# Optimization experiments

Measured on AMD Instinct MI355X. Metric: run time of the kernel, lower is better.

Reference implementation:

```python
import jax, jax.numpy as jnp
import numpy as np

GROUPSIZE = 128
IN_F, OUT_F = 4096, 11008
TOKENS = 512


def setup_inputs() -> dict:
    key = jax.random.key(0)
    k1, k2, k3, k4, k5 = jax.random.split(key, 5)
    x = jax.random.normal(k1, (TOKENS, IN_F), dtype=jnp.float32)
    # packed 4-bit codes: two nibbles per byte, stored as int32 in [0, 256)
    qweight = jax.random.randint(k2, (OUT_F * IN_F // 2,), 0, 256, dtype=jnp.int32)
    n_groups = OUT_F * IN_F // GROUPSIZE
    scales = jax.random.uniform(k3, (n_groups, 1), dtype=jnp.float32) * 0.02 + 1e-3
    zeros = jax.random.uniform(k4, (n_groups, 1), dtype=jnp.float32) * 15.0
    bias = jax.random.normal(k5, (OUT_F,), dtype=jnp.float32)
    return {"x": x, "qweight": qweight, "scales": scales, "zeros": zeros, "bias": bias}


def _dequant_w4(qweight, scales, zeros, dtype):
    # python_decompress: high nibble then low nibble, each in [0,16)
    hi = (qweight >> 4) % 16
    lo = qweight % 16
    codes = jnp.stack([hi, lo], axis=-1).reshape(-1, GROUPSIZE).astype(dtype)
    # group-wise dequant: (code - zero) * scale, zeros/scales are (n_groups, 1)
    w = (codes - zeros.astype(dtype)) * scales.astype(dtype)
    return w.reshape(OUT_F, IN_F)


def reference(x, qweight, scales, zeros, bias):
    w = _dequant_w4(qweight, scales, zeros, x.dtype)  # [out, in]
    return x @ w.T + bias
```

## Files before the change

kernel.cpp:

```cpp
#include <hip/hip_runtime.h>

#define GROUPSIZE 128
#define IN_F 4096
#define OUT_F 11008
#define TOKENS 512
#define N_GROUPS (OUT_F * IN_F / GROUPSIZE)
#define NGK (IN_F / GROUPSIZE)

#define BM 64
#define BN 128
#define BK 64
#define NTHREADS 256
#define NT_G (IN_F / BK)
#define NT_H (NT_G / 2)
#define NTILES_N (OUT_F / BN)

typedef _Float16 half8  __attribute__((ext_vector_type(8)));
typedef _Float16 half2v __attribute__((ext_vector_type(2)));
typedef float    f32x4  __attribute__((ext_vector_type(4)));
typedef int      ivec4  __attribute__((ext_vector_type(4)));

__device__ __forceinline__ int swz(int r, int k) {
    return ((r << 6) + k) ^ ((r & 7) << 3);
}

__device__ __forceinline__ void glds16(const _Float16* g, _Float16* l) {
    __builtin_amdgcn_global_load_lds(
        (const __attribute__((address_space(1))) void*)g,
        (__attribute__((address_space(3))) void*)l, 16, 0, 0);
}

__device__ __forceinline__ unsigned pack4(ivec4 q) {
    unsigned p01 = __builtin_amdgcn_perm((unsigned)q[1], (unsigned)q[0], 0x0C0C0400u);
    unsigned p23 = __builtin_amdgcn_perm((unsigned)q[3], (unsigned)q[2], 0x0C0C0400u);
    return __builtin_amdgcn_perm(p23, p01, 0x05040100u);
}

__device__ __forceinline__ half8 dqp(unsigned p, uint2 sz) {
    unsigned A4 = (p << 4) & 0xF0F0F0F0u;
    unsigned Bn =  p       & 0xF0F0F0F0u;
    unsigned t01 = __builtin_amdgcn_perm(A4, Bn, 0x05010400u);
    unsigned t23 = __builtin_amdgcn_perm(A4, Bn, 0x07030602u);
    const unsigned k54 = 0x54545454u;
    unsigned u0 = __builtin_amdgcn_perm(t01, k54, 0x00050004u);
    unsigned u1 = __builtin_amdgcn_perm(t01, k54, 0x00070006u);
    unsigned u2 = __builtin_amdgcn_perm(t23, k54, 0x00050004u);
    unsigned u3 = __builtin_amdgcn_perm(t23, k54, 0x00070006u);
    half2v S  = __builtin_bit_cast(half2v, sz.x);
    half2v Bv = __builtin_bit_cast(half2v, sz.y);
    union { half8 h; half2v p2[4]; } r;
    r.p2[0] = __builtin_bit_cast(half2v, u0) * S + Bv;
    r.p2[1] = __builtin_bit_cast(half2v, u1) * S + Bv;
    r.p2[2] = __builtin_bit_cast(half2v, u2) * S + Bv;
    r.p2[3] = __builtin_bit_cast(half2v, u3) * S + Bv;
    return r.h;
}

__global__ __launch_bounds__(256)
void cvt_x_kernel(const float* __restrict__ x, _Float16* __restrict__ x16) {
    size_t i = ((size_t)blockIdx.x * 256 + threadIdx.x) * 8;
    f32x4 a = *(const f32x4*)(x + i);
    f32x4 b = *(const f32x4*)(x + i + 4);
    half8 h;
    h[0]=(_Float16)a[0]; h[1]=(_Float16)a[1]; h[2]=(_Float16)a[2]; h[3]=(_Float16)a[3];
    h[4]=(_Float16)b[0]; h[5]=(_Float16)b[1]; h[6]=(_Float16)b[2]; h[7]=(_Float16)b[3];
    *(half8*)(x16 + i) = h;
}

__global__ __launch_bounds__(256)
void szpack_kernel(const float* __restrict__ s, const float* __restrict__ z,
                   uint2* __restrict__ szt) {
    int g = blockIdx.x * 256 + threadIdx.x;
    if (g >= N_GROUPS) return;
    int row = g / NGK, gk = g % NGK;
    _Float16 S = (_Float16)s[g];
    _Float16 B = (_Float16)(-(64.0f + z[g]) * (float)S);
    unsigned short su = __builtin_bit_cast(unsigned short, S);
    unsigned short bu = __builtin_bit_cast(unsigned short, B);
    uint2 r;
    r.x = ((unsigned)su << 16) | su;
    r.y = ((unsigned)bu << 16) | bu;
    szt[(size_t)gk * OUT_F + row] = r;
}

__global__ __launch_bounds__(256)
void out_init_kernel(const float* __restrict__ bias, float* __restrict__ out) {
    size_t i = ((size_t)blockIdx.x * 256 + threadIdx.x) * 4;
    int col = (int)(i % OUT_F);
    *(f32x4*)(out + i) = *(const f32x4*)(bias + col);
}

__global__ __launch_bounds__(NTHREADS, 4)
void qlinear_main(const _Float16* __restrict__ x16,
                  const int*   __restrict__ qw,
                  const uint2* __restrict__ szt,
                  float*       __restrict__ out)
{
    __shared__ __align__(16) _Float16 As[2][BM * BK];
    __shared__ __align__(16) unsigned Qs[2][BN * BK / 8];

    const int bid = blockIdx.x;
    const int xcd = bid & 7;
    const int sgrp = bid >> 3;
    const int n_t = 11 * xcd + (sgrp >> 4);
    const int sub = sgrp & 15;
    const int m_t = sub & 7;
    const int kh  = sub >> 3;
    if (n_t >= NTILES_N) return;
    const int n0 = n_t * BN, m0 = m_t * BM;
    const int t0 = kh * NT_H;

    const int tid = threadIdx.x;
    const int wv = tid >> 6, ln = tid & 63;

    const int s8 = tid & 7, r0 = tid >> 3;
    const int* qg = qw + (size_t)(n0 + r0) * (IN_F / 2) + (size_t)t0 * 32 + s8 * 4;
    const int dwp = s8 ^ ((r0 >> 2) & 3);

    const int ar  = wv * 16 + (ln >> 3);
    const int gsw = (ln & 7) ^ ((ln >> 3) & 7);
    const _Float16* ag = x16 + (size_t)(m0 + ar) * IN_F + (size_t)t0 * BK + gsw * 8;

    const int wc2 = wv * 32;
    const int lr = ln & 15, ln4 = ln >> 4, lk8 = ln4 * 8, lk4 = ln4 * 4;
    int qrd[2][2];
#pragma unroll
    for (int j = 0; j < 2; ++j) {
        int row = wc2 + j * 16 + lr;
        int qx = (row >> 2) & 3;
#pragma unroll
        for (int kk = 0; kk < 2; ++kk)
            qrd[j][kk] = row * 8 + ((kk * 4 + ln4) ^ qx);
    }
    const int szrow = n0 + wc2 + lr;

    f32x4 acc[4][2];
#pragma unroll
    for (int i = 0; i < 4; ++i)
#pragma unroll
        for (int j = 0; j < 2; ++j)
            acc[i][j] = (f32x4){0.f, 0.f, 0.f, 0.f};

#define LOAD_Q(qs, tt) do {                                                 \
        _Pragma("unroll")                                                   \
        for (int j = 0; j < 4; ++j)                                         \
            qs[j] = *(const ivec4*)(qg + (size_t)j * 32 * (IN_F/2) + (tt) * 32); \
    } while (0)

#define STAGE_A(tt, buf) do {                                               \
        const _Float16* gp = ag + (size_t)(tt) * 64;                        \
        glds16(gp,            &As[buf][wv * 1024]);                         \
        glds16(gp + 8 * IN_F, &As[buf][wv * 1024 + 512]);                   \
    } while (0)

#define PACK_STORE(qs, buf) do {                                            \
        _Pragma("unroll")                                                   \
        for (int j = 0; j < 4; ++j)                                         \
            Qs[buf][(r0 + 32 * j) * 8 + dwp] = pack4(qs[j]);                \
    } while (0)

    uint2 szc0, szc1;

    auto mfma_phase = [&](int b) {
#pragma unroll
        for (int kk = 0; kk < 2; ++kk) {
            half8 af[4];
#pragma unroll
            for (int i = 0; i < 4; ++i)
                af[i] = *(const half8*)&As[b][swz(i * 16 + lr, kk * 32 + lk8)];
            {
                half8 bf = dqp(Qs[b][qrd[0][kk]], szc0);
#pragma unroll
                for (int i = 0; i < 4; ++i)
                    acc[i][0] = __builtin_amdgcn_mfma_f32_16x16x32_f16(af[i], bf, acc[i][0], 0, 0, 0);
            }
            {
                half8 bf = dqp(Qs[b][qrd[1][kk]], szc1);
#pragma unroll
                for (int i = 0; i < 4; ++i)
                    acc[i][1] = __builtin_amdgcn_mfma_f32_16x16x32_f16(af[i], bf, acc[i][1], 0, 0, 0);
            }
        }
    };

    ivec4 qr[4];
    {
        int gk0 = t0 >> 1;
        szc0 = szt[(size_t)gk0 * OUT_F + szrow];
        szc1 = szt[(size_t)gk0 * OUT_F + szrow + 16];
        STAGE_A(0, 0);
        LOAD_Q(qr, 0);
        PACK_STORE(qr, 0);
        asm volatile("s_waitcnt vmcnt(0) lgkmcnt(0)" ::: "memory");
        __builtin_amdgcn_s_barrier();
    }

    for (int t = 0; t < NT_H; ++t) {
        const int b = t & 1;
        const int tn = (t + 1 < NT_H) ? t + 1 : NT_H - 1;
        const int gkn = (t0 + tn) >> 1;
        uint2 szn0 = szt[(size_t)gkn * OUT_F + szrow];
        uint2 szn1 = szt[(size_t)gkn * OUT_F + szrow + 16];
        STAGE_A(tn, b ^ 1);
        LOAD_Q(qr, tn);
        mfma_phase(b);
        PACK_STORE(qr, b ^ 1);
        asm volatile("s_waitcnt lgkmcnt(0)" ::: "memory");
        __builtin_amdgcn_s_barrier();
        szc0 = szn0; szc1 = szn1;
    }

#pragma unroll
    for (int j = 0; j < 2; ++j) {
        const int col = n0 + wc2 + j * 16 + lr;
#pragma unroll
        for (int i = 0; i < 4; ++i) {
            const int rb = m0 + i * 16 + lk4;
#pragma unroll
            for (int r = 0; r < 4; ++r)
                atomicAdd(&out[(size_t)(rb + r) * OUT_F + col], acc[i][j][r]);
        }
    }
#undef LOAD_Q
#undef STAGE_A
#undef PACK_STORE
}

extern "C" void kernel_launch(void* const* d_in, const int* in_sizes, int n_in,
                              void* d_out, int out_size, void* d_ws, size_t ws_size,
                              hipStream_t stream) {
    const float* x      = (const float*)d_in[0];
    const int*   qw     = (const int*)d_in[1];
    const float* scales = (const float*)d_in[2];
    const float* zeros  = (const float*)d_in[3];
    const float* bias   = (const float*)d_in[4];
    float*       out    = (float*)d_out;

    _Float16* x16 = (_Float16*)d_ws;
    uint2*    szt = (uint2*)((char*)d_ws + (size_t)TOKENS * IN_F * 2);

    cvt_x_kernel<<<TOKENS * IN_F / (256 * 8), 256, 0, stream>>>(x, x16);
    szpack_kernel<<<(N_GROUPS + 255) / 256, 256, 0, stream>>>(scales, zeros, szt);
    out_init_kernel<<<TOKENS * OUT_F / (256 * 4), 256, 0, stream>>>(bias, out);

    qlinear_main<<<1408, NTHREADS, 0, stream>>>(x16, qw, szt, out);
}
```

Baseline: 256.9 us.

## Repack 4-bit weights into MFMA fragment layout and drop LDS staging

Adds a pre-pass that packs the int32 nibble codes into a compact per-tile layout matching the MFMA B-fragment, so the main kernel loads weights directly into registers instead of staging them through LDS. The main loop is unrolled by two with register double-buffering, and occupancy is raised to five blocks per CU. The aim is to cut global weight bytes read in the hot loop and remove LDS traffic and pack work. The price is an extra full pass over the int32 weights each call, plus extra workspace that falls back to a direct-load path when space is short.

```diff
diff --git a/kernel.cpp b/kernel.cpp
--- a/kernel.cpp
+++ b/kernel.cpp
@@ -15,10 +15,16 @@
 #define NT_H (NT_G / 2)
 #define NTILES_N (OUT_F / BN)
 
+#define WS_SZT_OFF ((size_t)TOKENS * IN_F * 2)
+#define WS_PQ_OFF  (WS_SZT_OFF + (size_t)N_GROUPS * 8)
+#define WS_NEEDED  (WS_PQ_OFF + (size_t)OUT_F * IN_F / 2)
+
 typedef _Float16 half8  __attribute__((ext_vector_type(8)));
 typedef _Float16 half2v __attribute__((ext_vector_type(2)));
 typedef float    f32x4  __attribute__((ext_vector_type(4)));
 typedef int      ivec4  __attribute__((ext_vector_type(4)));
+
+#define MEMFENCE() asm volatile("" ::: "memory")
 
 __device__ __forceinline__ int swz(int r, int k) {
     return ((r << 6) + k) ^ ((r & 7) << 3);
@@ -90,14 +96,25 @@
     *(f32x4*)(out + i) = *(const f32x4*)(bias + col);
 }
 
-__global__ __launch_bounds__(NTHREADS, 4)
+__global__ __launch_bounds__(256)
+void repack_q_kernel(const int* __restrict__ qw, unsigned* __restrict__ pq) {
+    unsigned tg = blockIdx.x * 256 + threadIdx.x;
+    ivec4 q = *(const ivec4*)(qw + (size_t)tg * 4);
+    unsigned ln4 = tg & 3, kk = (tg >> 2) & 1, ts = (tg >> 3) & 63;
+    unsigned row_g = tg >> 9;
+    unsigned nt = row_g >> 7, row = row_g & 127;
+    size_t O = ((size_t)(nt * 64 + ts)) * 1024 + ln4 * 256 + row * 2 + kk;
+    pq[O] = pack4(q);
+}
+
+template <int PACKED>
+__global__ __launch_bounds__(NTHREADS, 5)
 void qlinear_main(const _Float16* __restrict__ x16,
-                  const int*   __restrict__ qw,
+                  const void*  __restrict__ qsrc,
                   const uint2* __restrict__ szt,
                   float*       __restrict__ out)
 {
     __shared__ __align__(16) _Float16 As[2][BM * BK];
-    __shared__ __align__(16) unsigned Qs[2][BN * BK / 8];
 
     const int bid = blockIdx.x;
     const int xcd = bid & 7;
@@ -113,26 +130,29 @@
     const int tid = threadIdx.x;
     const int wv = tid >> 6, ln = tid & 63;
 
-    const int s8 = tid & 7, r0 = tid >> 3;
-    const int* qg = qw + (size_t)(n0 + r0) * (IN_F / 2) + (size_t)t0 * 32 + s8 * 4;
-    const int dwp = s8 ^ ((r0 >> 2) & 3);
-
     const int ar  = wv * 16 + (ln >> 3);
     const int gsw = (ln & 7) ^ ((ln >> 3) & 7);
     const _Float16* ag = x16 + (size_t)(m0 + ar) * IN_F + (size_t)t0 * BK + gsw * 8;
 
     const int wc2 = wv * 32;
     const int lr = ln & 15, ln4 = ln >> 4, lk8 = ln4 * 8, lk4 = ln4 * 4;
-    int qrd[2][2];
-#pragma unroll
-    for (int j = 0; j < 2; ++j) {
-        int row = wc2 + j * 16 + lr;
-        int qx = (row >> 2) & 3;
-#pragma unroll
-        for (int kk = 0; kk < 2; ++kk)
-            qrd[j][kk] = row * 8 + ((kk * 4 + ln4) ^ qx);
-    }
     const int szrow = n0 + wc2 + lr;
+
+    const uint2* qp0 = nullptr; const uint2* qp1 = nullptr;
+    const int *qf0 = nullptr, *qf1 = nullptr, *qf2 = nullptr, *qf3 = nullptr;
+    if constexpr (PACKED) {
+        const unsigned* Pq = (const unsigned*)qsrc;
+        size_t base = ((size_t)(n_t * 64 + t0)) * 1024 + (size_t)ln4 * 256
+                    + (size_t)(wc2 + lr) * 2;
+        qp0 = (const uint2*)(Pq + base);
+        qp1 = (const uint2*)(Pq + base + 32);
+    } else {
+        const int* qw = (const int*)qsrc;
+        const int* b = qw + (size_t)(n0 + wc2 + lr) * (IN_F / 2)
+                     + (size_t)t0 * 32 + ln4 * 4;
+        qf0 = b; qf1 = b + 16;
+        qf2 = b + (size_t)16 * (IN_F / 2); qf3 = qf2 + 16;
+    }
 
     f32x4 acc[4][2];
 #pragma unroll
@@ -141,73 +161,82 @@
         for (int j = 0; j < 2; ++j)
             acc[i][j] = (f32x4){0.f, 0.f, 0.f, 0.f};
 
-#define LOAD_Q(qs, tt) do {                                                 \
-        _Pragma("unroll")                                                   \
-        for (int j = 0; j < 4; ++j)                                         \
-            qs[j] = *(const ivec4*)(qg + (size_t)j * 32 * (IN_F/2) + (tt) * 32); \
-    } while (0)
-
-#define STAGE_A(tt, buf) do {                                               \
-        const _Float16* gp = ag + (size_t)(tt) * 64;                        \
-        glds16(gp,            &As[buf][wv * 1024]);                         \
-        glds16(gp + 8 * IN_F, &As[buf][wv * 1024 + 512]);                   \
-    } while (0)
-
-#define PACK_STORE(qs, buf) do {                                            \
-        _Pragma("unroll")                                                   \
-        for (int j = 0; j < 4; ++j)                                         \
-            Qs[buf][(r0 + 32 * j) * 8 + dwp] = pack4(qs[j]);                \
-    } while (0)
-
-    uint2 szc0, szc1;
-
-    auto mfma_phase = [&](int b) {
+#define STAGE_A(tt, buf) do {                                      \
+        const _Float16* gp = ag + (size_t)(tt) * 64;               \
+        glds16(gp,            &As[buf][wv * 1024]);                \
+        glds16(gp + 8 * IN_F, &As[buf][wv * 1024 + 512]);          \
+        MEMFENCE();    \
+    } while (0)
+
+#define LOAD_QP(a0, a1, tt) do {                                   \
+        a0 = qp0[(size_t)(tt) * 512]; a1 = qp1[(size_t)(tt) * 512]; \
+    } while (0)
+
+#define LOAD_QF(fr, tt) do {                                       \
+        fr[0] = *(const ivec4*)(qf0 + (tt) * 32);                  \
+        fr[1] = *(const ivec4*)(qf1 + (tt) * 32);                  \
+        fr[2] = *(const ivec4*)(qf2 + (tt) * 32);                  \
+        fr[3] = *(const ivec4*)(qf3 + (tt) * 32);                  \
+    } while (0)
+
+    auto mfma_phase = [&](int b, uint2 q0, uint2 q1,
+                          ivec4 f0, ivec4 f1, ivec4 f2, ivec4 f3,
+                          uint2 sz0, uint2 sz1) {
 #pragma unroll
         for (int kk = 0; kk < 2; ++kk) {
             half8 af[4];
 #pragma unroll
             for (int i = 0; i < 4; ++i)
                 af[i] = *(const half8*)&As[b][swz(i * 16 + lr, kk * 32 + lk8)];
-            {
-                half8 bf = dqp(Qs[b][qrd[0][kk]], szc0);
-#pragma unroll
-                for (int i = 0; i < 4; ++i)
-                    acc[i][0] = __builtin_amdgcn_mfma_f32_16x16x32_f16(af[i], bf, acc[i][0], 0, 0, 0);
-            }
-            {
-                half8 bf = dqp(Qs[b][qrd[1][kk]], szc1);
-#pragma unroll
-                for (int i = 0; i < 4; ++i)
-                    acc[i][1] = __builtin_amdgcn_mfma_f32_16x16x32_f16(af[i], bf, acc[i][1], 0, 0, 0);
-            }
+            unsigned p0, p1;
+            if constexpr (PACKED) { p0 = kk ? q0.y : q0.x; p1 = kk ? q1.y : q1.x; }
+            else { p0 = pack4(kk ? f1 : f0); p1 = pack4(kk ? f3 : f2); }
+            half8 bf0 = dqp(p0, sz0);
+#pragma unroll
+            for (int i = 0; i < 4; ++i)
+                acc[i][0] = __builtin_amdgcn_mfma_f32_16x16x32_f16(af[i], bf0, acc[i][0], 0, 0, 0);
+            half8 bf1 = dqp(p1, sz1);
+#pragma unroll
+            for (int i = 0; i < 4; ++i)
+                acc[i][1] = __builtin_amdgcn_mfma_f32_16x16x32_f16(af[i], bf1, acc[i][1], 0, 0, 0);
         }
     };
 
-    ivec4 qr[4];
+#define WAITBAR() do {                                                   \
+        asm volatile("s_waitcnt vmcnt(0) lgkmcnt(0)" ::: "memory");      \
+        __builtin_amdgcn_s_barrier();                                    \
+    } while (0)
+
+    uint2 qE0{}, qE1{}, qO0{}, qO1{};
+    ivec4 fE[4] = {}, fO[4] = {};
+    uint2 szc0, szc1, szn0, szn1;
     {
-        int gk0 = t0 >> 1;
+        const int gk0 = t0 >> 1;
         szc0 = szt[(size_t)gk0 * OUT_F + szrow];
         szc1 = szt[(size_t)gk0 * OUT_F + szrow + 16];
         STAGE_A(0, 0);
-        LOAD_Q(qr, 0);
-        PACK_STORE(qr, 0);
-        asm volatile("s_waitcnt vmcnt(0) lgkmcnt(0)" ::: "memory");
-        __builtin_amdgcn_s_barrier();
-    }
-
-    for (int t = 0; t < NT_H; ++t) {
-        const int b = t & 1;
-        const int tn = (t + 1 < NT_H) ? t + 1 : NT_H - 1;
-        const int gkn = (t0 + tn) >> 1;
-        uint2 szn0 = szt[(size_t)gkn * OUT_F + szrow];
-        uint2 szn1 = szt[(size_t)gkn * OUT_F + szrow + 16];
-        STAGE_A(tn, b ^ 1);
-        LOAD_Q(qr, tn);
-        mfma_phase(b);
-        PACK_STORE(qr, b ^ 1);
-        asm volatile("s_waitcnt lgkmcnt(0)" ::: "memory");
-        __builtin_amdgcn_s_barrier();
-        szc0 = szn0; szc1 = szn1;
+        if constexpr (PACKED) LOAD_QP(qE0, qE1, 0); else LOAD_QF(fE, 0);
+        WAITBAR();
+    }
+
+    for (int t = 0; t < NT_H; t += 2) {
+        {
+            STAGE_A(t + 1, 1);
+            if constexpr (PACKED) LOAD_QP(qO0, qO1, t + 1); else LOAD_QF(fO, t + 1);
+            mfma_phase(0, qE0, qE1, fE[0], fE[1], fE[2], fE[3], szc0, szc1);
+            WAITBAR();
+        }
+        {
+            const int tn = (t + 2 < NT_H) ? t + 2 : NT_H - 1;
+            STAGE_A(tn, 0);
+            if constexpr (PACKED) LOAD_QP(qE0, qE1, tn); else LOAD_QF(fE, tn);
+            const int gkn = (t0 + tn) >> 1;
+            szn0 = szt[(size_t)gkn * OUT_F + szrow];
+            szn1 = szt[(size_t)gkn * OUT_F + szrow + 16];
+            mfma_phase(1, qO0, qO1, fO[0], fO[1], fO[2], fO[3], szc0, szc1);
+            WAITBAR();
+            szc0 = szn0; szc1 = szn1;
+        }
     }
 
 #pragma unroll
@@ -221,9 +250,10 @@
                 atomicAdd(&out[(size_t)(rb + r) * OUT_F + col], acc[i][j][r]);
         }
     }
-#undef LOAD_Q
 #undef STAGE_A
-#undef PACK_STORE
+#undef LOAD_QP
+#undef LOAD_QF
+#undef WAITBAR
 }
 
 extern "C" void kernel_launch(void* const* d_in, const int* in_sizes, int n_in,
@@ -236,12 +266,19 @@
     const float* bias   = (const float*)d_in[4];
     float*       out    = (float*)d_out;
 
-    _Float16* x16 = (_Float16*)d_ws;
-    uint2*    szt = (uint2*)((char*)d_ws + (size_t)TOKENS * IN_F * 2);
+    char* ws = (char*)d_ws;
+    _Float16* x16 = (_Float16*)ws;
+    uint2*    szt = (uint2*)(ws + WS_SZT_OFF);
 
     cvt_x_kernel<<<TOKENS * IN_F / (256 * 8), 256, 0, stream>>>(x, x16);
     szpack_kernel<<<(N_GROUPS + 255) / 256, 256, 0, stream>>>(scales, zeros, szt);
     out_init_kernel<<<TOKENS * OUT_F / (256 * 4), 256, 0, stream>>>(bias, out);
 
-    qlinear_main<<<1408, NTHREADS, 0, stream>>>(x16, qw, szt, out);
-}
+    if (ws_size >= WS_NEEDED) {
+        unsigned* pq = (unsigned*)(ws + WS_PQ_OFF);
+        repack_q_kernel<<<(OUT_F * IN_F / 8) / 256, 256, 0, stream>>>(qw, pq);
+        qlinear_main<1><<<1408, NTHREADS, 0, stream>>>(x16, pq, szt, out);
+    } else {
+        qlinear_main<0><<<1408, NTHREADS, 0, stream>>>(x16, qw, szt, out);
+    }
+}
```

After: 258.0 us. No clear change (+0.4%).
